# Kernel optimization log

Measured on AMD Instinct MI355X. Metric: run time of the kernel, lower is better.

## Reference

```python
import jax, jax.numpy as jnp
import numpy as np

N_NODES = 100000
N_EDGES = 3200000
IN_DIM = 128
EMB = 32
NUM_GRAPHS = 256


def setup_inputs() -> dict:
    key = jax.random.key(0)
    ks = jax.random.split(key, 7)
    x = jax.random.normal(ks[0], (N_NODES, IN_DIM), dtype=jnp.float32)
    edge_index = jax.random.randint(ks[1], (2, N_EDGES), 0, N_NODES, dtype=jnp.int64)
    batch_index = jnp.sort(jax.random.randint(ks[2], (N_NODES,), 0, NUM_GRAPHS, dtype=jnp.int64))
    W1 = jax.random.normal(ks[3], (IN_DIM, EMB), dtype=jnp.float32) * (1.0 / np.sqrt(IN_DIM))
    b1 = jax.random.normal(ks[4], (EMB,), dtype=jnp.float32) * 0.01
    Wout = jax.random.normal(ks[5], (2 * EMB, 1), dtype=jnp.float32) * (1.0 / np.sqrt(2 * EMB))
    bout = jax.random.normal(ks[6], (1,), dtype=jnp.float32) * 0.01
    return {"x": x, "edge_index": edge_index, "batch_index": batch_index,
            "W1": W1, "b1": b1, "Wout": Wout, "bout": bout}


def gcn_conv(x, edge_index, W, b):
    """PyG GCNConv: add self-loops, symmetric deg^-1/2 normalization, XW, scatter-add, +bias."""
    N = x.shape[0]
    xw = x @ W  # [N, out]
    src, dst = edge_index[0], edge_index[1]
    # degree includes self-loop (+1)
    deg = jax.ops.segment_sum(jnp.ones(src.shape[0], dtype=xw.dtype), dst, num_segments=N) + 1.0
    dinv = jax.lax.rsqrt(deg)  # deg >= 1 so safe
    norm = dinv[src] * dinv[dst]  # [E]
    msg = xw[src] * norm[:, None]  # [E, out]
    agg = jax.ops.segment_sum(msg, dst, num_segments=N)
    # self-loop contribution: dinv[i]^2 * xw[i]
    agg = agg + xw * (dinv * dinv)[:, None]
    return agg + b


def reference(x, edge_index, batch_index, W1, b1, Wout, bout):
    h = gcn_conv(x, edge_index, W1, b1)           # [N, EMB]
    h = jnp.tanh(h)
    sums = jax.ops.segment_sum(h, batch_index, num_segments=NUM_GRAPHS)   # global_add_pool
    counts = jax.ops.segment_sum(jnp.ones((h.shape[0],), dtype=h.dtype), batch_index, num_segments=NUM_GRAPHS)
    means = sums / jnp.maximum(counts, 1.0)[:, None]                       # global_mean_pool
    pooled = jnp.concatenate([sums, means], axis=1)  # [G, 2*EMB]
    return pooled @ Wout + bout                      # [G, 1]
```

## Files before the change

### kernel.cpp

```cpp
#include <hip/hip_runtime.h>
#include <hip/hip_fp16.h>

#define N_NODES    100000
#define N_EDGES    3200000
#define IN_DIM     128
#define EMB        32
#define NUM_GRAPHS 256

#define FB         1024
#define NODES_PB   128
#define NBUCKETS   782
#define FB_B       512
#define FB_EPB     6250
#define NCHUNK     16
#define CHROWS     32
#define XW_BLOCKS  1563
#define CAP        5632

typedef _Float16 half8 __attribute__((ext_vector_type(8)));
typedef float floatx4 __attribute__((ext_vector_type(4)));

__global__ __launch_bounds__(512) void k_hist(const int* __restrict__ ei,
                                              int* __restrict__ bhist) {
    __shared__ int h[FB];
    int t = threadIdx.x;
    for (int i = t; i < FB; i += 512) h[i] = 0;
    __syncthreads();
    int e0 = blockIdx.x * FB_EPB;
    for (int e = e0 + t; e < e0 + FB_EPB; e += 512)
        atomicAdd(&h[ei[N_EDGES + e] >> 7], 1);
    __syncthreads();
    for (int i = t; i < FB; i += 512) bhist[blockIdx.x * FB + i] = h[i];
}

__global__ __launch_bounds__(512) void k_part(const int* __restrict__ bhist,
                                              int* __restrict__ part,
                                              const int* __restrict__ batch,
                                              float* __restrict__ sums,
                                              float* __restrict__ counts) {
    int j = blockIdx.x, t = threadIdx.x;
    if (j == NCHUNK) {
        for (int i = t; i < NUM_GRAPHS * EMB; i += 512) sums[i] = 0.f;
        if (t < NUM_GRAPHS) {
            int lo = 0, hi = N_NODES;
            while (lo < hi) { int mid = (lo + hi) >> 1; if (batch[mid] < t) lo = mid + 1; else hi = mid; }
            int a = lo;
            lo = 0; hi = N_NODES;
            int g1 = t + 1;
            while (lo < hi) { int mid = (lo + hi) >> 1; if (batch[mid] < g1) lo = mid + 1; else hi = mid; }
            counts[t] = (float)(lo - a);
        }
        return;
    }
    int row0 = j * CHROWS;
    for (int b = t; b < FB; b += 512) {
        int acc = 0;
#pragma unroll 8
        for (int i = 0; i < CHROWS; ++i) acc += bhist[(row0 + i) * FB + b];
        part[j * FB + b] = acc;
    }
}

__global__ __launch_bounds__(1024) void k_mid(const int* __restrict__ bhist,
                                              const int* __restrict__ part,
                                              int* __restrict__ bbase,
                                              int* __restrict__ cbase) {
    __shared__ int ts[FB];
    int b = threadIdx.x;
    int j = blockIdx.x;
    int tot = 0;
#pragma unroll
    for (int k = 0; k < NCHUNK; ++k) tot += part[k * FB + b];
    ts[b] = tot;
    __syncthreads();
    for (int off = 1; off < FB; off <<= 1) {
        int u = (b >= off) ? ts[b - off] : 0;
        __syncthreads();
        ts[b] += u;
        __syncthreads();
    }
    int cb = ts[b] - tot;
    if (j == 0) {
        cbase[b] = cb;
        if (b == 0) cbase[FB] = N_EDGES;
    }
    int run = cb;
    for (int k = 0; k < j; ++k) run += part[k * FB + b];
    int row0 = j * CHROWS;
    for (int i = 0; i < CHROWS; ++i) {
        int h = bhist[(row0 + i) * FB + b];
        bbase[(row0 + i) * FB + b] = run;
        run += h;
    }
}

__global__ __launch_bounds__(512) void k_fill(const int* __restrict__ ei,
                                              const int* __restrict__ bhist,
                                              const int* __restrict__ bbase,
                                              unsigned int* __restrict__ recs) {
    __shared__ unsigned int staged[FB_EPB];
    __shared__ int dpos[FB_EPB];
    __shared__ int hd[FB];
    __shared__ int cur[FB];
    __shared__ int ts[512];
    int t = threadIdx.x;
    int rowoff = blockIdx.x * FB;
    for (int i = t; i < FB; i += 512) hd[i] = bhist[rowoff + i];
    __syncthreads();
    int v0 = hd[2 * t], v1 = hd[2 * t + 1];
    int tot = v0 + v1;
    ts[t] = tot;
    __syncthreads();
    for (int off = 1; off < 512; off <<= 1) {
        int u = (t >= off) ? ts[t - off] : 0;
        __syncthreads();
        ts[t] += u;
        __syncthreads();
    }
    int lb0 = ts[t] - tot;
    int lb1 = lb0 + v0;
    cur[2 * t] = lb0;
    cur[2 * t + 1] = lb1;
    hd[2 * t]     = bbase[rowoff + 2 * t]     - lb0;
    hd[2 * t + 1] = bbase[rowoff + 2 * t + 1] - lb1;
    __syncthreads();
    int e0 = blockIdx.x * FB_EPB;
    for (int e = e0 + t; e < e0 + FB_EPB; e += 512) {
        int s = ei[e];
        int d = ei[N_EDGES + e];
        int b = d >> 7;
        int lpos = atomicAdd(&cur[b], 1);
        staged[lpos] = ((unsigned int)(d & 127) << 24) | (unsigned int)s;
        dpos[lpos] = lpos + hd[b];
    }
    __syncthreads();
    for (int j = t; j < FB_EPB; j += 512)
        recs[dpos[j]] = staged[j];
}

__global__ __launch_bounds__(512) void k_fill2(const unsigned int* __restrict__ recs,
                                               const int* __restrict__ cbase,
                                               int* __restrict__ edge_src,
                                               int* __restrict__ rowstart,
                                               float* __restrict__ dinv) {
    __shared__ unsigned int lbuf[CAP];
    __shared__ int h2[NODES_PB], cur2[NODES_PB], sc[NODES_PB];
    int t = threadIdx.x, b = blockIdx.x;
    if (t < NODES_PB) h2[t] = 0;
    __syncthreads();
    int seg0 = cbase[b];
    int cnt = cbase[b + 1] - seg0;
    for (int j = t; j < cnt; j += 512) {
        unsigned int r = recs[seg0 + j];
        if (j < CAP) lbuf[j] = r;
        atomicAdd(&h2[r >> 24], 1);
    }
    __syncthreads();
    int v = 0;
    if (t < NODES_PB) { v = h2[t]; sc[t] = v; }
    __syncthreads();
    for (int off = 1; off < NODES_PB; off <<= 1) {
        int u = 0;
        if (t < NODES_PB && t >= off) u = sc[t - off];
        __syncthreads();
        if (t < NODES_PB) sc[t] += u;
        __syncthreads();
    }
    int node0 = b << 7;
    if (t < NODES_PB) {
        int excl = sc[t] - v;
        cur2[t] = excl;
        int node = node0 + t;
        if (node < N_NODES) {
            rowstart[node] = seg0 + excl;
            dinv[node] = rsqrtf((float)v + 1.0f);
        }
    }
    if (b == 0 && t == 0) rowstart[N_NODES] = N_EDGES;
    __syncthreads();
    for (int j = t; j < cnt; j += 512) {
        unsigned int r = (j < CAP) ? lbuf[j] : recs[seg0 + j];
        int p = atomicAdd(&cur2[r >> 24], 1);
        edge_src[seg0 + p] = (int)(r & 0x00FFFFFF);
    }
}

__global__ __launch_bounds__(256) void k_xw(const float* __restrict__ x,
                                            const float* __restrict__ W1,
                                            const float* __restrict__ dinv,
                                            __half* __restrict__ xwh) {
    __shared__ _Float16 Wh[IN_DIM * (EMB + 1)];
    for (int i = threadIdx.x; i < IN_DIM * EMB; i += 256)
        Wh[(i >> 5) * (EMB + 1) + (i & 31)] = (_Float16)W1[i];
    __syncthreads();
    int wave = threadIdx.x >> 6;
    int lane = threadIdx.x & 63;
    int m = lane & 15, quad = lane >> 4;
    int row0 = (blockIdx.x * 4 + wave) * 16;
    if (row0 >= N_NODES) return;
    half8 bfrag[2][4];
#pragma unroll
    for (int nt = 0; nt < 2; ++nt)
#pragma unroll
        for (int ks = 0; ks < 4; ++ks)
#pragma unroll
            for (int j = 0; j < 8; ++j)
                bfrag[nt][ks][j] = Wh[(ks * 32 + quad * 8 + j) * (EMB + 1) + nt * 16 + m];
    const float* xr = x + (size_t)(row0 + m) * IN_DIM + quad * 8;
    floatx4 c0 = {0.f, 0.f, 0.f, 0.f}, c1 = {0.f, 0.f, 0.f, 0.f};
#pragma unroll
    for (int ks = 0; ks < 4; ++ks) {
        float4 a0 = *(const float4*)(xr + ks * 32);
        float4 a1 = *(const float4*)(xr + ks * 32 + 4);
        half8 af;
        af[0] = (_Float16)a0.x; af[1] = (_Float16)a0.y;
        af[2] = (_Float16)a0.z; af[3] = (_Float16)a0.w;
        af[4] = (_Float16)a1.x; af[5] = (_Float16)a1.y;
        af[6] = (_Float16)a1.z; af[7] = (_Float16)a1.w;
        c0 = __builtin_amdgcn_mfma_f32_16x16x32_f16(af, bfrag[0][ks], c0, 0, 0, 0);
        c1 = __builtin_amdgcn_mfma_f32_16x16x32_f16(af, bfrag[1][ks], c1, 0, 0, 0);
    }
#pragma unroll
    for (int r = 0; r < 4; ++r) {
        int ro = row0 + quad * 4 + r;
        float di = dinv[ro];
        xwh[(size_t)ro * EMB + m]      = __float2half(c0[r] * di);
        xwh[(size_t)ro * EMB + 16 + m] = __float2half(c1[r] * di);
    }
}

template<int K>
__device__ __forceinline__ void gstep(const int* __restrict__ es,
                                      const __half2* __restrict__ rows,
                                      int cc, int e, float& a0, float& a1) {
    int s[K];
    float2 f[K];
#pragma unroll
    for (int k = 0; k < K; ++k) s[k] = es[e + k];
#pragma unroll
    for (int k = 0; k < K; ++k) f[k] = __half22float2(rows[s[k] * 16 + cc]);
#pragma unroll
    for (int k = 0; k < K; ++k) { a0 += f[k].x; a1 += f[k].y; }
}

__global__ __launch_bounds__(256) void k_gather(const __half* __restrict__ xws,
                                                const float* __restrict__ dinv,
                                                const int* __restrict__ rowstart,
                                                const int* __restrict__ edge_src,
                                                const int* __restrict__ batch,
                                                const float* __restrict__ b1,
                                                float* __restrict__ sums) {
    const __half2* rows = (const __half2*)xws;
    int grp = threadIdx.x >> 4;
    int cc  = threadIdx.x & 15;
    int i = blockIdx.x * 16 + grp;
    float di = dinv[i];
    int e0 = rowstart[i], e1 = rowstart[i + 1];
    float a0 = 0.f, a1 = 0.f;
    int e = e0;
    for (; e + 16 <= e1; e += 16) gstep<16>(edge_src, rows, cc, e, a0, a1);
    if (e + 8 <= e1) { gstep<8>(edge_src, rows, cc, e, a0, a1); e += 8; }
    if (e + 4 <= e1) { gstep<4>(edge_src, rows, cc, e, a0, a1); e += 4; }
    if (e + 2 <= e1) { gstep<2>(edge_src, rows, cc, e, a0, a1); e += 2; }
    if (e < e1)      { gstep<1>(edge_src, rows, cc, e, a0, a1); }
    float2 fs = __half22float2(rows[i * 16 + cc]);
    float2 bb = *(const float2*)(b1 + 2 * cc);
    float h0 = tanhf((a0 + fs.x) * di + bb.x);
    float h1 = tanhf((a1 + fs.y) * di + bb.y);

    __shared__ float hs[16][EMB];
    __shared__ int gb[16];
    *(float2*)&hs[grp][2 * cc] = make_float2(h0, h1);
    if (cc == 0) gb[grp] = batch[i];
    __syncthreads();
    if (threadIdx.x < 32) {
        int col = threadIdx.x;
        int rr = 0;
        while (rr < 16) {
            int g0 = gb[rr];
            float a = hs[rr][col];
            int r2 = rr + 1;
            while (r2 < 16 && gb[r2] == g0) { a += hs[r2][col]; ++r2; }
            atomicAdd(&sums[g0 * EMB + col], a);
            rr = r2;
        }
    }
}

__global__ __launch_bounds__(64) void k_out(const float* __restrict__ sums,
                                            const float* __restrict__ counts,
                                            const float* __restrict__ Wout,
                                            const float* __restrict__ bout,
                                            float* __restrict__ out) {
    int g = blockIdx.x * 64 + threadIdx.x;
    if (g >= NUM_GRAPHS) return;
    float inv = 1.0f / fmaxf(counts[g], 1.0f);
    float acc = bout[0];
#pragma unroll
    for (int c = 0; c < EMB; ++c) {
        float s = sums[g * EMB + c];
        acc += s * Wout[c] + s * inv * Wout[EMB + c];
    }
    out[g] = acc;
}

extern "C" void kernel_launch(void* const* d_in, const int* in_sizes, int n_in,
                              void* d_out, int out_size, void* d_ws, size_t ws_size,
                              hipStream_t stream) {
    const float* x     = (const float*)d_in[0];
    const int*   ei    = (const int*)d_in[1];
    const int*   batch = (const int*)d_in[2];
    const float* W1    = (const float*)d_in[3];
    const float* b1    = (const float*)d_in[4];
    const float* Wout  = (const float*)d_in[5];
    const float* bout  = (const float*)d_in[6];
    float* out = (float*)d_out;

    char* ws = (char*)d_ws;
    __half* xwh        = (__half*)ws;       ws += (size_t)N_NODES * EMB * sizeof(__half);
    unsigned int* recs = (unsigned int*)ws; ws += (size_t)N_EDGES * sizeof(int);
    int*   edge_src    = (int*)ws;          ws += (size_t)N_EDGES * sizeof(int);
    int*   rowstart    = (int*)ws;          ws += (size_t)(N_NODES + 4) * sizeof(int);
    float* dinv        = (float*)ws;        ws += (size_t)N_NODES * sizeof(float);
    int*   cbase       = (int*)ws;          ws += (FB + 2) * sizeof(int);
    float* sums        = (float*)ws;        ws += (size_t)NUM_GRAPHS * EMB * sizeof(float);
    float* counts      = (float*)ws;

    int* bhist = edge_src;
    int* part  = edge_src + (size_t)FB_B * FB;
    int* bbase = part + (size_t)NCHUNK * FB;

    k_hist  <<<FB_B, 512, 0, stream>>>(ei, bhist);
    k_part  <<<NCHUNK + 1, 512, 0, stream>>>(bhist, part, batch, sums, counts);
    k_mid   <<<NCHUNK, 1024, 0, stream>>>(bhist, part, bbase, cbase);
    k_fill  <<<FB_B, 512, 0, stream>>>(ei, bhist, bbase, recs);
    k_fill2 <<<NBUCKETS, 512, 0, stream>>>(recs, cbase, edge_src, rowstart, dinv);
    k_xw    <<<XW_BLOCKS, 256, 0, stream>>>(x, W1, dinv, xwh);
    k_gather<<<N_NODES / 16, 256, 0, stream>>>(xwh, dinv, rowstart, edge_src, batch, b1, sums);
    k_out   <<<(NUM_GRAPHS + 63) / 64, 64, 0, stream>>>(sums, counts, Wout, bout, out);
}
```

Baseline: 203.5 us.

## Fuse per-bucket CSR scatter into gather kernel using LDS-resident source lists

The second fill pass no longer writes a sorted edge_src array to global memory. It becomes a degree-only kernel, and the new gather kernel re-reads each bucket's records, sorts the source indices into LDS, and gathers from there, spilling to a global overflow buffer only when a bucket exceeds capacity. The gather also pre-reduces graph sums in shared memory for up to four graphs per block before issuing global atomics. This removes one global write and one read of the edge array, but the gather now runs 782 large blocks of 512 threads with about 23 KB of LDS each, which can lower occupancy and latency hiding for the random row loads.

```diff
diff --git a/kernel.cpp b/kernel.cpp
--- a/kernel.cpp
+++ b/kernel.cpp
@@ -16,6 +16,7 @@
 #define CHROWS     32
 #define XW_BLOCKS  1563
 #define CAP        5632
+#define GMAX       4
 
 typedef _Float16 half8 __attribute__((ext_vector_type(8)));
 typedef float floatx4 __attribute__((ext_vector_type(4)));
@@ -138,23 +139,18 @@
         recs[dpos[j]] = staged[j];
 }
 
-__global__ __launch_bounds__(512) void k_fill2(const unsigned int* __restrict__ recs,
-                                               const int* __restrict__ cbase,
-                                               int* __restrict__ edge_src,
-                                               int* __restrict__ rowstart,
-                                               float* __restrict__ dinv) {
-    __shared__ unsigned int lbuf[CAP];
-    __shared__ int h2[NODES_PB], cur2[NODES_PB], sc[NODES_PB];
+__global__ __launch_bounds__(512) void k_deg(const unsigned int* __restrict__ recs,
+                                             const int* __restrict__ cbase,
+                                             int* __restrict__ rowstart,
+                                             float* __restrict__ dinv) {
+    __shared__ int h2[NODES_PB], sc[NODES_PB];
     int t = threadIdx.x, b = blockIdx.x;
     if (t < NODES_PB) h2[t] = 0;
     __syncthreads();
     int seg0 = cbase[b];
     int cnt = cbase[b + 1] - seg0;
-    for (int j = t; j < cnt; j += 512) {
-        unsigned int r = recs[seg0 + j];
-        if (j < CAP) lbuf[j] = r;
-        atomicAdd(&h2[r >> 24], 1);
-    }
+    for (int j = t; j < cnt; j += 512)
+        atomicAdd(&h2[recs[seg0 + j] >> 24], 1);
     __syncthreads();
     int v = 0;
     if (t < NODES_PB) { v = h2[t]; sc[t] = v; }
@@ -166,23 +162,14 @@
         if (t < NODES_PB) sc[t] += u;
         __syncthreads();
     }
-    int node0 = b << 7;
     if (t < NODES_PB) {
-        int excl = sc[t] - v;
-        cur2[t] = excl;
-        int node = node0 + t;
+        int node = (b << 7) + t;
         if (node < N_NODES) {
-            rowstart[node] = seg0 + excl;
+            rowstart[node] = seg0 + sc[t] - v;
             dinv[node] = rsqrtf((float)v + 1.0f);
         }
     }
     if (b == 0 && t == 0) rowstart[N_NODES] = N_EDGES;
-    __syncthreads();
-    for (int j = t; j < cnt; j += 512) {
-        unsigned int r = (j < CAP) ? lbuf[j] : recs[seg0 + j];
-        int p = atomicAdd(&cur2[r >> 24], 1);
-        edge_src[seg0 + p] = (int)(r & 0x00FFFFFF);
-    }
 }
 
 __global__ __launch_bounds__(256) void k_xw(const float* __restrict__ x,
@@ -229,61 +216,105 @@
     }
 }
 
-template<int K>
-__device__ __forceinline__ void gstep(const int* __restrict__ es,
-                                      const __half2* __restrict__ rows,
+template<int K, bool OVF>
+__device__ __forceinline__ void lstep(const int* __restrict__ srt,
+                                      const unsigned int* __restrict__ ovf,
+                                      int seg0, const __half2* __restrict__ rows,
                                       int cc, int e, float& a0, float& a1) {
     int s[K];
     float2 f[K];
 #pragma unroll
-    for (int k = 0; k < K; ++k) s[k] = es[e + k];
-#pragma unroll
-    for (int k = 0; k < K; ++k) f[k] = __half22float2(rows[s[k] * 16 + cc]);
+    for (int k = 0; k < K; ++k) {
+        int idx = e + k;
+        if (OVF) s[k] = (idx < CAP) ? srt[idx] : (int)ovf[seg0 + idx];
+        else     s[k] = srt[idx];
+    }
+#pragma unroll
+    for (int k = 0; k < K; ++k) f[k] = __half22float2(rows[(size_t)s[k] * 16 + cc]);
 #pragma unroll
     for (int k = 0; k < K; ++k) { a0 += f[k].x; a1 += f[k].y; }
 }
 
-__global__ __launch_bounds__(256) void k_gather(const __half* __restrict__ xws,
-                                                const float* __restrict__ dinv,
-                                                const int* __restrict__ rowstart,
-                                                const int* __restrict__ edge_src,
-                                                const int* __restrict__ batch,
-                                                const float* __restrict__ b1,
-                                                float* __restrict__ sums) {
-    const __half2* rows = (const __half2*)xws;
-    int grp = threadIdx.x >> 4;
-    int cc  = threadIdx.x & 15;
-    int i = blockIdx.x * 16 + grp;
-    float di = dinv[i];
-    int e0 = rowstart[i], e1 = rowstart[i + 1];
-    float a0 = 0.f, a1 = 0.f;
+template<bool OVF>
+__device__ __forceinline__ void node_gather(const int* __restrict__ srt,
+                                            const unsigned int* __restrict__ ovf,
+                                            int seg0, const __half2* __restrict__ rows,
+                                            int cc, int e0, int e1, float& a0, float& a1) {
     int e = e0;
-    for (; e + 16 <= e1; e += 16) gstep<16>(edge_src, rows, cc, e, a0, a1);
-    if (e + 8 <= e1) { gstep<8>(edge_src, rows, cc, e, a0, a1); e += 8; }
-    if (e + 4 <= e1) { gstep<4>(edge_src, rows, cc, e, a0, a1); e += 4; }
-    if (e + 2 <= e1) { gstep<2>(edge_src, rows, cc, e, a0, a1); e += 2; }
-    if (e < e1)      { gstep<1>(edge_src, rows, cc, e, a0, a1); }
-    float2 fs = __half22float2(rows[i * 16 + cc]);
+    for (; e + 16 <= e1; e += 16) lstep<16, OVF>(srt, ovf, seg0, rows, cc, e, a0, a1);
+    if (e + 8 <= e1) { lstep<8, OVF>(srt, ovf, seg0, rows, cc, e, a0, a1); e += 8; }
+    if (e + 4 <= e1) { lstep<4, OVF>(srt, ovf, seg0, rows, cc, e, a0, a1); e += 4; }
+    if (e + 2 <= e1) { lstep<2, OVF>(srt, ovf, seg0, rows, cc, e, a0, a1); e += 2; }
+    if (e < e1)      { lstep<1, OVF>(srt, ovf, seg0, rows, cc, e, a0, a1); }
+}
+
+__global__ __launch_bounds__(512) void k_fg(const unsigned int* __restrict__ recs,
+                                            const int* __restrict__ rowstart,
+                                            const __half* __restrict__ xwh,
+                                            const int* __restrict__ batch,
+                                            const float* __restrict__ b1,
+                                            float* __restrict__ sums,
+                                            unsigned int* __restrict__ ovf) {
+    __shared__ int srt[CAP];
+    __shared__ int rs[NODES_PB + 1];
+    __shared__ int cur[NODES_PB];
+    __shared__ float gsum[GMAX][EMB];
+    __shared__ int gfirst;
+    int t = threadIdx.x, b = blockIdx.x;
+    int node0 = b << 7;
+    if (t <= NODES_PB)
+        rs[t] = (node0 + t <= N_NODES) ? rowstart[node0 + t] : N_EDGES;
+    if (t < GMAX * EMB) ((float*)gsum)[t] = 0.f;
+    if (t == 0) gfirst = batch[node0];
+    __syncthreads();
+    if (t < NODES_PB) cur[t] = rs[t];
+    int seg0 = rs[0];
+    int cnt = rs[NODES_PB] - seg0;
+    __syncthreads();
+    for (int j = t; j < cnt; j += 512) {
+        unsigned int r = recs[seg0 + j];
+        int gp = atomicAdd(&cur[r >> 24], 1);
+        int lp = gp - seg0;
+        int s = (int)(r & 0x00FFFFFF);
+        if (lp < CAP) srt[lp] = s;
+        else          ovf[gp] = (unsigned int)s;
+    }
+    __syncthreads();
+    bool has_ovf = (cnt > CAP);
+    const __half2* rows = (const __half2*)xwh;
+    int grp = t >> 4, cc = t & 15;
     float2 bb = *(const float2*)(b1 + 2 * cc);
-    float h0 = tanhf((a0 + fs.x) * di + bb.x);
-    float h1 = tanhf((a1 + fs.y) * di + bb.y);
-
-    __shared__ float hs[16][EMB];
-    __shared__ int gb[16];
-    *(float2*)&hs[grp][2 * cc] = make_float2(h0, h1);
-    if (cc == 0) gb[grp] = batch[i];
-    __syncthreads();
-    if (threadIdx.x < 32) {
-        int col = threadIdx.x;
-        int rr = 0;
-        while (rr < 16) {
-            int g0 = gb[rr];
-            float a = hs[rr][col];
-            int r2 = rr + 1;
-            while (r2 < 16 && gb[r2] == g0) { a += hs[r2][col]; ++r2; }
-            atomicAdd(&sums[g0 * EMB + col], a);
-            rr = r2;
+    int gf = gfirst;
+#pragma unroll 1
+    for (int rep = 0; rep < 4; ++rep) {
+        int li = rep * 32 + grp;
+        int i = node0 + li;
+        if (i < N_NODES) {
+            int e0 = rs[li] - seg0, e1 = rs[li + 1] - seg0;
+            float a0 = 0.f, a1 = 0.f;
+            if (has_ovf) node_gather<true >(srt, ovf, seg0, rows, cc, e0, e1, a0, a1);
+            else         node_gather<false>(srt, ovf, seg0, rows, cc, e0, e1, a0, a1);
+            float di = rsqrtf((float)(e1 - e0) + 1.0f);
+            float2 fs = __half22float2(rows[(size_t)i * 16 + cc]);
+            float h0 = tanhf((a0 + fs.x) * di + bb.x);
+            float h1 = tanhf((a1 + fs.y) * di + bb.y);
+            int g = batch[i];
+            int gl = g - gf;
+            if (gl >= 0 && gl < GMAX) {
+                atomicAdd(&gsum[gl][2 * cc], h0);
+                atomicAdd(&gsum[gl][2 * cc + 1], h1);
+            } else {
+                atomicAdd(&sums[g * EMB + 2 * cc], h0);
+                atomicAdd(&sums[g * EMB + 2 * cc + 1], h1);
+            }
         }
+    }
+    __syncthreads();
+    if (t < GMAX * EMB) {
+        int gl = t >> 5, col = t & 31;
+        float v = gsum[gl][col];
+        int g = gf + gl;
+        if (v != 0.f && g < NUM_GRAPHS) atomicAdd(&sums[g * EMB + col], v);
     }
 }
 
@@ -319,23 +350,23 @@
     char* ws = (char*)d_ws;
     __half* xwh        = (__half*)ws;       ws += (size_t)N_NODES * EMB * sizeof(__half);
     unsigned int* recs = (unsigned int*)ws; ws += (size_t)N_EDGES * sizeof(int);
-    int*   edge_src    = (int*)ws;          ws += (size_t)N_EDGES * sizeof(int);
+    unsigned int* escr = (unsigned int*)ws; ws += (size_t)N_EDGES * sizeof(int);
     int*   rowstart    = (int*)ws;          ws += (size_t)(N_NODES + 4) * sizeof(int);
     float* dinv        = (float*)ws;        ws += (size_t)N_NODES * sizeof(float);
     int*   cbase       = (int*)ws;          ws += (FB + 2) * sizeof(int);
     float* sums        = (float*)ws;        ws += (size_t)NUM_GRAPHS * EMB * sizeof(float);
     float* counts      = (float*)ws;
 
-    int* bhist = edge_src;
-    int* part  = edge_src + (size_t)FB_B * FB;
+    int* bhist = (int*)escr;
+    int* part  = bhist + (size_t)FB_B * FB;
     int* bbase = part + (size_t)NCHUNK * FB;
 
-    k_hist  <<<FB_B, 512, 0, stream>>>(ei, bhist);
-    k_part  <<<NCHUNK + 1, 512, 0, stream>>>(bhist, part, batch, sums, counts);
-    k_mid   <<<NCHUNK, 1024, 0, stream>>>(bhist, part, bbase, cbase);
-    k_fill  <<<FB_B, 512, 0, stream>>>(ei, bhist, bbase, recs);
-    k_fill2 <<<NBUCKETS, 512, 0, stream>>>(recs, cbase, edge_src, rowstart, dinv);
-    k_xw    <<<XW_BLOCKS, 256, 0, stream>>>(x, W1, dinv, xwh);
-    k_gather<<<N_NODES / 16, 256, 0, stream>>>(xwh, dinv, rowstart, edge_src, batch, b1, sums);
-    k_out   <<<(NUM_GRAPHS + 63) / 64, 64, 0, stream>>>(sums, counts, Wout, bout, out);
-}
+    k_hist <<<FB_B, 512, 0, stream>>>(ei, bhist);
+    k_part <<<NCHUNK + 1, 512, 0, stream>>>(bhist, part, batch, sums, counts);
+    k_mid  <<<NCHUNK, 1024, 0, stream>>>(bhist, part, bbase, cbase);
+    k_fill <<<FB_B, 512, 0, stream>>>(ei, bhist, bbase, recs);
+    k_deg  <<<NBUCKETS, 512, 0, stream>>>(recs, cbase, rowstart, dinv);
+    k_xw   <<<XW_BLOCKS, 256, 0, stream>>>(x, W1, dinv, xwh);
+    k_fg   <<<NBUCKETS, 512, 0, stream>>>(recs, rowstart, xwh, batch, b1, sums, escr);
+    k_out  <<<(NUM_GRAPHS + 63) / 64, 64, 0, stream>>>(sums, counts, Wout, bout, out);
+}
```

Measured after the change: 208.0 us. 1.02x slower.
